# Performance work log

Hardware: AMD Instinct MI355X
Metric: run time of the kernel (lower is better)

The kernel has to match this reference:

```python
import jax, jax.numpy as jnp
import numpy as np

B, N, E, D = 4, 50000, 800000, 64


def setup_inputs() -> dict:
    key = jax.random.key(0)
    k_h, k_e, k_w1, k_w2 = jax.random.split(key, 4)
    s = 1.0 / np.sqrt(D)  # glorot-ish scale for 64x64 linear weights
    return {
        "t": jnp.zeros((1,), jnp.float32),
        "h": jax.random.normal(k_h, (B, N, D), jnp.float32),
        "edge_index": jax.random.randint(k_e, (2, E), 0, N, jnp.int32),
        "W1": jax.random.normal(k_w1, (D, D), jnp.float32) * s,
        "b1": jnp.zeros((D,), jnp.float32),
        "W2": jax.random.normal(k_w2, (D, D), jnp.float32) * s,
        "b2": jnp.zeros((D,), jnp.float32),
    }


def _gcn(x, row, col, norm, W, b, n_nodes):
    # x: (B, N, D). PyG GCNConv: linear (no bias) -> normalized gather/scatter -> +bias
    xw = jnp.einsum("bnd,de->bne", x, W)
    msg = xw[:, row, :] * norm[None, :, None]          # (B, E+N, D)
    agg = jax.vmap(lambda m: jax.ops.segment_sum(m, col, num_segments=n_nodes))(msg)
    return agg + b


def reference(t, h, edge_index, W1, b1, W2, b2):
    n_nodes = h.shape[1]
    loop = jnp.arange(n_nodes, dtype=edge_index.dtype)
    # add self-loops (PyG GCNConv default)
    row = jnp.concatenate([edge_index[0], loop])  # source nodes
    col = jnp.concatenate([edge_index[1], loop])  # target nodes
    # symmetric normalization D^{-1/2} (A+I) D^{-1/2}; degree counted on targets
    deg = jax.ops.segment_sum(jnp.ones_like(row, dtype=h.dtype), col, num_segments=n_nodes)
    dis = jnp.where(deg > 0, jax.lax.rsqrt(deg), 0.0)
    norm = dis[row] * dis[col]
    h = jnp.tanh(_gcn(h, row, col, norm, W1, b1, n_nodes))
    h = jnp.tanh(_gcn(h, row, col, norm, W2, b2, n_nodes))
    return h
```

## Files before the change

kernel.cpp:

```cpp
#include <hip/hip_runtime.h>
#include <math.h>

#define B_ 4
#define N_ 50000
#define E_ 800000
#define D_ 64
#define M_ (B_*N_)

#define LIN_BLKS_ (M_/64)
#define FILL_BLKS_ ((E_+255)/256)
#define CNT_BLKS_ ((E_/4+255)/256)

typedef _Float16 h4 __attribute__((ext_vector_type(4)));
typedef _Float16 h8 __attribute__((ext_vector_type(8)));
typedef float    f4 __attribute__((ext_vector_type(4)));

__device__ __forceinline__ void wfrag_one(const float* __restrict__ W, h8* __restrict__ Wf, int fid) {
  int khalf = fid >> 8, rem = fid & 255, tt = rem >> 6, lane = rem & 63;
  int kq = lane >> 4, m = lane & 15;
  h8 v;
#pragma unroll
  for (int j = 0; j < 8; j++) {
    int k = khalf * 32 + kq * 8 + j;
    v[j] = (_Float16)W[k * 64 + tt * 16 + m];
  }
  Wf[fid] = v;
}

__global__ __launch_bounds__(256) void k_count(const int4* __restrict__ col4, int* __restrict__ cnt,
                                               const float* __restrict__ W1, const float* __restrict__ W2,
                                               h8* __restrict__ Wf1, h8* __restrict__ Wf2) {
  if (blockIdx.x >= CNT_BLKS_) {
    int fa = (blockIdx.x - CNT_BLKS_) * 256 + threadIdx.x;
    if (fa < 512) wfrag_one(W1, Wf1, fa);
    else          wfrag_one(W2, Wf2, fa - 512);
    return;
  }
  int e = blockIdx.x * 256 + threadIdx.x;
  if (e < E_ / 4) {
    int4 c = col4[e];
    atomicAdd(&cnt[c.x], 1);
    atomicAdd(&cnt[c.y], 1);
    atomicAdd(&cnt[c.z], 1);
    atomicAdd(&cnt[c.w], 1);
  }
}

__global__ __launch_bounds__(1024) void k_scan(const int* __restrict__ cnt,
                                               float* __restrict__ dis,
                                               int* __restrict__ off, int* __restrict__ cur,
                                               int* __restrict__ gbase) {
  __shared__ int sd[1024];
  __shared__ int base_s;
  int i = blockIdx.x * 1024 + threadIdx.x;
  int v = (i < N_) ? cnt[i] : 0;
  if (i < N_) dis[i] = 1.0f / sqrtf((float)(v + 1));
  sd[threadIdx.x] = v;
  __syncthreads();
  for (int s = 1; s < 1024; s <<= 1) {
    int t = (threadIdx.x >= s) ? sd[threadIdx.x - s] : 0;
    __syncthreads();
    sd[threadIdx.x] += t;
    __syncthreads();
  }
  if (threadIdx.x == 1023) base_s = atomicAdd(gbase, sd[1023]);
  __syncthreads();
  if (i < N_) {
    off[i] = base_s + sd[threadIdx.x] - v;
    cur[i] = 0;
  }
}

template<int IN_F16>
__device__ __forceinline__ void linear_wave(const void* __restrict__ Xv, const h8* __restrict__ Wf,
                                            _Float16* __restrict__ Y, int wv, int lane) {
  int m = lane & 15, kq = lane >> 4;
  size_t r0 = (size_t)wv * 16;
  h8 a0, a1;
  if constexpr (IN_F16) {
    const _Float16* xr = (const _Float16*)Xv + (r0 + m) * 64 + kq * 8;
    a0 = *(const h8*)(xr);
    a1 = *(const h8*)(xr + 32);
  } else {
    const float* xr = (const float*)Xv + (r0 + m) * 64 + kq * 8;
    f4 f0 = *(const f4*)(xr);
    f4 f1 = *(const f4*)(xr + 4);
    f4 f2 = *(const f4*)(xr + 32);
    f4 f3 = *(const f4*)(xr + 36);
#pragma unroll
    for (int j = 0; j < 4; j++) {
      a0[j] = (_Float16)f0[j]; a0[j + 4] = (_Float16)f1[j];
      a1[j] = (_Float16)f2[j]; a1[j + 4] = (_Float16)f3[j];
    }
  }
  f4 acc[4];
#pragma unroll
  for (int t = 0; t < 4; t++) {
    h8 b0 = Wf[t * 64 + lane];
    h8 b1 = Wf[256 + t * 64 + lane];
    f4 c = {0.f, 0.f, 0.f, 0.f};
    c = __builtin_amdgcn_mfma_f32_16x16x32_f16(a0, b0, c, 0, 0, 0);
    c = __builtin_amdgcn_mfma_f32_16x16x32_f16(a1, b1, c, 0, 0, 0);
    acc[t] = c;
  }
  int b  = (int)(r0 / N_);
  int n0 = (int)(r0 - (size_t)b * N_);
#pragma unroll
  for (int t = 0; t < 4; t++) {
#pragma unroll
    for (int r = 0; r < 4; r++) {
      int n = n0 + kq * 4 + r;
      Y[(size_t)n * 256 + b * 64 + t * 16 + m] = (_Float16)acc[t][r];
    }
  }
}

__global__ __launch_bounds__(256) void k_fill_lin1(const int* __restrict__ row, const int* __restrict__ col,
                                                   const int* __restrict__ off, int* __restrict__ cur,
                                                   const float* __restrict__ dis, int2* __restrict__ em,
                                                   const float* __restrict__ h, const h8* __restrict__ Wf1,
                                                   _Float16* __restrict__ xw) {
  if (blockIdx.x < LIN_BLKS_) {
    int wv = blockIdx.x * 4 + (threadIdx.x >> 6);
    linear_wave<0>(h, Wf1, xw, wv, threadIdx.x & 63);
    return;
  }
  int e = (blockIdx.x - LIN_BLKS_) * 256 + threadIdx.x;
  if (e < E_) {
    int c = col[e], r = row[e];
    int p = off[c] + atomicAdd(&cur[c], 1);
    float w = dis[r] * dis[c];
    em[p] = make_int2(r << 9, __float_as_int(w));
  }
}

__global__ __launch_bounds__(256) void k_linear2(const _Float16* __restrict__ X, const h8* __restrict__ Wf,
                                                 _Float16* __restrict__ Y) {
  int wv = blockIdx.x * 4 + (threadIdx.x >> 6);
  linear_wave<1>(X, Wf, Y, wv, threadIdx.x & 63);
}

template<int OUT_F16>
__global__ __launch_bounds__(512) void k_agg(const _Float16* __restrict__ xw,
                                             const int* __restrict__ off,
                                             const int* __restrict__ cnt,
                                             const int2* __restrict__ em,
                                             const float* __restrict__ bias,
                                             void* __restrict__ outv) {
  int node = blockIdx.x * 8 + (threadIdx.x >> 6);
  int lane = threadIdx.x & 63;
  const char* xb = (const char*)xw + (size_t)(lane * 8);
  int s0  = __builtin_amdgcn_readfirstlane(off[node]);
  int deg = __builtin_amdgcn_readfirstlane(cnt[node]);
  int e0  = s0 + deg;
  float sw = 1.0f / (float)(deg + 1);
  h4 sv = *(const h4*)(xb + ((size_t)node << 9));
  f4 acc = __builtin_convertvector(sv, f4) * sw;
#define EDGE_(mm) do { \
    h4 v_ = *(const h4*)(xb + (unsigned)(mm).x); \
    acc += __builtin_convertvector(v_, f4) * __int_as_float((mm).y); \
  } while (0)
  int j = s0;
  for (; j + 8 <= e0; j += 8) {
    int2 m0 = em[j],     m1 = em[j + 1], m2 = em[j + 2], m3 = em[j + 3];
    int2 m4 = em[j + 4], m5 = em[j + 5], m6 = em[j + 6], m7 = em[j + 7];
    EDGE_(m0); EDGE_(m1); EDGE_(m2); EDGE_(m3);
    EDGE_(m4); EDGE_(m5); EDGE_(m6); EDGE_(m7);
  }
  for (; j < e0; ++j) { int2 mm = em[j]; EDGE_(mm); }
#undef EDGE_
  int b  = lane >> 4;
  int d0 = (lane & 15) * 4;
  f4 bb = *(const f4*)(bias + d0);
  float r0 = tanhf(acc.x + bb.x);
  float r1 = tanhf(acc.y + bb.y);
  float r2 = tanhf(acc.z + bb.z);
  float r3 = tanhf(acc.w + bb.w);
  if constexpr (OUT_F16) {
    h4 o;
    o[0] = (_Float16)r0; o[1] = (_Float16)r1;
    o[2] = (_Float16)r2; o[3] = (_Float16)r3;
    *(h4*)((_Float16*)outv + ((size_t)b * N_ + node) * 64 + d0) = o;
  } else {
    f4 r = {r0, r1, r2, r3};
    *(f4*)((float*)outv + ((size_t)b * N_ + node) * 64 + d0) = r;
  }
}

extern "C" void kernel_launch(void* const* d_in, const int* in_sizes, int n_in,
                              void* d_out, int out_size, void* d_ws, size_t ws_size,
                              hipStream_t stream) {
  const float* h  = (const float*)d_in[1];
  const int*   ei = (const int*)d_in[2];
  const float* W1 = (const float*)d_in[3];
  const float* b1 = (const float*)d_in[4];
  const float* W2 = (const float*)d_in[5];
  const float* b2 = (const float*)d_in[6];
  float* out = (float*)d_out;
  const int* row = ei;
  const int* col = ei + E_;

  char* p = (char*)d_ws;
  _Float16* xw = (_Float16*)p; p += (size_t)M_ * D_ * sizeof(_Float16);
  int2* em  = (int2*)p;   p += (size_t)E_ * sizeof(int2);
  int*  cnt = (int*)p;    p += (size_t)N_ * sizeof(int);
  int*  gbase = (int*)p;  p += 4 * sizeof(int);
  int*  off = (int*)p;    p += (size_t)N_ * sizeof(int);
  int*  cur = (int*)p;    p += (size_t)N_ * sizeof(int);
  float* dis = (float*)p; p += (size_t)N_ * sizeof(float);
  h8*   Wf1 = (h8*)p;     p += 512 * sizeof(h8);
  h8*   Wf2 = (h8*)p;     p += 512 * sizeof(h8);
  _Float16* h1 = (_Float16*)d_out;

  hipMemsetAsync(cnt, 0, (N_ + 4) * sizeof(int), stream);

  k_count<<<CNT_BLKS_ + 4, 256, 0, stream>>>((const int4*)col, cnt, W1, W2, Wf1, Wf2);
  k_scan<<<(N_ + 1023) / 1024, 1024, 0, stream>>>(cnt, dis, off, cur, gbase);
  k_fill_lin1<<<LIN_BLKS_ + FILL_BLKS_, 256, 0, stream>>>(row, col, off, cur, dis, em, h, Wf1, xw);
  k_agg<1><<<N_ / 8, 512, 0, stream>>>(xw, off, cnt, em, b1, h1);
  k_linear2<<<M_ / 64, 256, 0, stream>>>(h1, Wf2, xw);
  k_agg<0><<<N_ / 8, 512, 0, stream>>>(xw, off, cnt, em, b2, out);
}
```

Measured before the change: 326.1 us.

## Reuse count atomics as CSR ranks and aggregate two nodes per wave

```diff
diff --git a/kernel.cpp b/kernel.cpp
--- a/kernel.cpp
+++ b/kernel.cpp
@@ -28,6 +28,7 @@
 }
 
 __global__ __launch_bounds__(256) void k_count(const int4* __restrict__ col4, int* __restrict__ cnt,
+                                               int4* __restrict__ rank4,
                                                const float* __restrict__ W1, const float* __restrict__ W2,
                                                h8* __restrict__ Wf1, h8* __restrict__ Wf2) {
   if (blockIdx.x >= CNT_BLKS_) {
@@ -39,17 +40,18 @@
   int e = blockIdx.x * 256 + threadIdx.x;
   if (e < E_ / 4) {
     int4 c = col4[e];
-    atomicAdd(&cnt[c.x], 1);
-    atomicAdd(&cnt[c.y], 1);
-    atomicAdd(&cnt[c.z], 1);
-    atomicAdd(&cnt[c.w], 1);
+    int4 r;
+    r.x = atomicAdd(&cnt[c.x], 1);
+    r.y = atomicAdd(&cnt[c.y], 1);
+    r.z = atomicAdd(&cnt[c.z], 1);
+    r.w = atomicAdd(&cnt[c.w], 1);
+    rank4[e] = r;
   }
 }
 
 __global__ __launch_bounds__(1024) void k_scan(const int* __restrict__ cnt,
                                                float* __restrict__ dis,
-                                               int* __restrict__ off, int* __restrict__ cur,
-                                               int* __restrict__ gbase) {
+                                               int* __restrict__ off, int* __restrict__ gbase) {
   __shared__ int sd[1024];
   __shared__ int base_s;
   int i = blockIdx.x * 1024 + threadIdx.x;
@@ -65,10 +67,7 @@
   }
   if (threadIdx.x == 1023) base_s = atomicAdd(gbase, sd[1023]);
   __syncthreads();
-  if (i < N_) {
-    off[i] = base_s + sd[threadIdx.x] - v;
-    cur[i] = 0;
-  }
+  if (i < N_) off[i] = base_s + sd[threadIdx.x] - v;
 }
 
 template<int IN_F16>
@@ -116,7 +115,7 @@
 }
 
 __global__ __launch_bounds__(256) void k_fill_lin1(const int* __restrict__ row, const int* __restrict__ col,
-                                                   const int* __restrict__ off, int* __restrict__ cur,
+                                                   const int* __restrict__ off, const int* __restrict__ rank,
                                                    const float* __restrict__ dis, int2* __restrict__ em,
                                                    const float* __restrict__ h, const h8* __restrict__ Wf1,
                                                    _Float16* __restrict__ xw) {
@@ -128,7 +127,7 @@
   int e = (blockIdx.x - LIN_BLKS_) * 256 + threadIdx.x;
   if (e < E_) {
     int c = col[e], r = row[e];
-    int p = off[c] + atomicAdd(&cur[c], 1);
+    int p = off[c] + rank[e];
     float w = dis[r] * dis[c];
     em[p] = make_int2(r << 9, __float_as_int(w));
   }
@@ -147,44 +146,98 @@
                                              const int2* __restrict__ em,
                                              const float* __restrict__ bias,
                                              void* __restrict__ outv) {
-  int node = blockIdx.x * 8 + (threadIdx.x >> 6);
+  int wid  = blockIdx.x * 8 + (threadIdx.x >> 6);
   int lane = threadIdx.x & 63;
+  int na = wid * 2, nb = na + 1;
   const char* xb = (const char*)xw + (size_t)(lane * 8);
-  int s0  = __builtin_amdgcn_readfirstlane(off[node]);
-  int deg = __builtin_amdgcn_readfirstlane(cnt[node]);
-  int e0  = s0 + deg;
-  float sw = 1.0f / (float)(deg + 1);
-  h4 sv = *(const h4*)(xb + ((size_t)node << 9));
-  f4 acc = __builtin_convertvector(sv, f4) * sw;
-#define EDGE_(mm) do { \
+  int sa = __builtin_amdgcn_readfirstlane(off[na]);
+  int da = __builtin_amdgcn_readfirstlane(cnt[na]);
+  int sb = __builtin_amdgcn_readfirstlane(off[nb]);
+  int db = __builtin_amdgcn_readfirstlane(cnt[nb]);
+  int ea = sa + da, eb = sb + db;
+  float swa = 1.0f / (float)(da + 1);
+  float swb = 1.0f / (float)(db + 1);
+  h4 sva = *(const h4*)(xb + ((size_t)na << 9));
+  h4 svb = *(const h4*)(xb + ((size_t)nb << 9));
+  f4 acca = __builtin_convertvector(sva, f4) * swa;
+  f4 accb = __builtin_convertvector(svb, f4) * swb;
+#define EDGE_(mm, acc) do { \
     h4 v_ = *(const h4*)(xb + (unsigned)(mm).x); \
     acc += __builtin_convertvector(v_, f4) * __int_as_float((mm).y); \
   } while (0)
-  int j = s0;
-  for (; j + 8 <= e0; j += 8) {
-    int2 m0 = em[j],     m1 = em[j + 1], m2 = em[j + 2], m3 = em[j + 3];
-    int2 m4 = em[j + 4], m5 = em[j + 5], m6 = em[j + 6], m7 = em[j + 7];
-    EDGE_(m0); EDGE_(m1); EDGE_(m2); EDGE_(m3);
-    EDGE_(m4); EDGE_(m5); EDGE_(m6); EDGE_(m7);
-  }
-  for (; j < e0; ++j) { int2 mm = em[j]; EDGE_(mm); }
+#define BATCH8_(j, acc) do { \
+    int2 m0 = em[j],     m1 = em[(j)+1], m2 = em[(j)+2], m3 = em[(j)+3]; \
+    int2 m4 = em[(j)+4], m5 = em[(j)+5], m6 = em[(j)+6], m7 = em[(j)+7]; \
+    EDGE_(m0, acc); EDGE_(m1, acc); EDGE_(m2, acc); EDGE_(m3, acc); \
+    EDGE_(m4, acc); EDGE_(m5, acc); EDGE_(m6, acc); EDGE_(m7, acc); \
+  } while (0)
+  int ja = sa, jb = sb;
+  while (ja + 8 <= ea && jb + 8 <= eb) {
+    int2 a0 = em[ja],     a1 = em[ja + 1], a2 = em[ja + 2], a3 = em[ja + 3];
+    int2 a4 = em[ja + 4], a5 = em[ja + 5], a6 = em[ja + 6], a7 = em[ja + 7];
+    int2 b0 = em[jb],     b1 = em[jb + 1], b2 = em[jb + 2], b3 = em[jb + 3];
+    int2 b4 = em[jb + 4], b5 = em[jb + 5], b6 = em[jb + 6], b7 = em[jb + 7];
+    h4 va0 = *(const h4*)(xb + (unsigned)a0.x);
+    h4 va1 = *(const h4*)(xb + (unsigned)a1.x);
+    h4 va2 = *(const h4*)(xb + (unsigned)a2.x);
+    h4 va3 = *(const h4*)(xb + (unsigned)a3.x);
+    h4 va4 = *(const h4*)(xb + (unsigned)a4.x);
+    h4 va5 = *(const h4*)(xb + (unsigned)a5.x);
+    h4 va6 = *(const h4*)(xb + (unsigned)a6.x);
+    h4 va7 = *(const h4*)(xb + (unsigned)a7.x);
+    h4 vb0 = *(const h4*)(xb + (unsigned)b0.x);
+    h4 vb1 = *(const h4*)(xb + (unsigned)b1.x);
+    h4 vb2 = *(const h4*)(xb + (unsigned)b2.x);
+    h4 vb3 = *(const h4*)(xb + (unsigned)b3.x);
+    h4 vb4 = *(const h4*)(xb + (unsigned)b4.x);
+    h4 vb5 = *(const h4*)(xb + (unsigned)b5.x);
+    h4 vb6 = *(const h4*)(xb + (unsigned)b6.x);
+    h4 vb7 = *(const h4*)(xb + (unsigned)b7.x);
+    acca += __builtin_convertvector(va0, f4) * __int_as_float(a0.y);
+    acca += __builtin_convertvector(va1, f4) * __int_as_float(a1.y);
+    acca += __builtin_convertvector(va2, f4) * __int_as_float(a2.y);
+    acca += __builtin_convertvector(va3, f4) * __int_as_float(a3.y);
+    acca += __builtin_convertvector(va4, f4) * __int_as_float(a4.y);
+    acca += __builtin_convertvector(va5, f4) * __int_as_float(a5.y);
+    acca += __builtin_convertvector(va6, f4) * __int_as_float(a6.y);
+    acca += __builtin_convertvector(va7, f4) * __int_as_float(a7.y);
+    accb += __builtin_convertvector(vb0, f4) * __int_as_float(b0.y);
+    accb += __builtin_convertvector(vb1, f4) * __int_as_float(b1.y);
+    accb += __builtin_convertvector(vb2, f4) * __int_as_float(b2.y);
+    accb += __builtin_convertvector(vb3, f4) * __int_as_float(b3.y);
+    accb += __builtin_convertvector(vb4, f4) * __int_as_float(b4.y);
+    accb += __builtin_convertvector(vb5, f4) * __int_as_float(b5.y);
+    accb += __builtin_convertvector(vb6, f4) * __int_as_float(b6.y);
+    accb += __builtin_convertvector(vb7, f4) * __int_as_float(b7.y);
+    ja += 8; jb += 8;
+  }
+  while (ja + 8 <= ea) { BATCH8_(ja, acca); ja += 8; }
+  while (jb + 8 <= eb) { BATCH8_(jb, accb); jb += 8; }
+  for (; ja < ea; ++ja) { int2 mm = em[ja]; EDGE_(mm, acca); }
+  for (; jb < eb; ++jb) { int2 mm = em[jb]; EDGE_(mm, accb); }
+#undef BATCH8_
 #undef EDGE_
   int b  = lane >> 4;
   int d0 = (lane & 15) * 4;
   f4 bb = *(const f4*)(bias + d0);
-  float r0 = tanhf(acc.x + bb.x);
-  float r1 = tanhf(acc.y + bb.y);
-  float r2 = tanhf(acc.z + bb.z);
-  float r3 = tanhf(acc.w + bb.w);
-  if constexpr (OUT_F16) {
-    h4 o;
-    o[0] = (_Float16)r0; o[1] = (_Float16)r1;
-    o[2] = (_Float16)r2; o[3] = (_Float16)r3;
-    *(h4*)((_Float16*)outv + ((size_t)b * N_ + node) * 64 + d0) = o;
-  } else {
-    f4 r = {r0, r1, r2, r3};
-    *(f4*)((float*)outv + ((size_t)b * N_ + node) * 64 + d0) = r;
-  }
+#define STORE_(acc, node) do { \
+    float r0 = tanhf((acc).x + bb.x); \
+    float r1 = tanhf((acc).y + bb.y); \
+    float r2 = tanhf((acc).z + bb.z); \
+    float r3 = tanhf((acc).w + bb.w); \
+    if constexpr (OUT_F16) { \
+      h4 o; \
+      o[0] = (_Float16)r0; o[1] = (_Float16)r1; \
+      o[2] = (_Float16)r2; o[3] = (_Float16)r3; \
+      *(h4*)((_Float16*)outv + ((size_t)b * N_ + (node)) * 64 + d0) = o; \
+    } else { \
+      f4 r = {r0, r1, r2, r3}; \
+      *(f4*)((float*)outv + ((size_t)b * N_ + (node)) * 64 + d0) = r; \
+    } \
+  } while (0)
+  STORE_(acca, na);
+  STORE_(accb, nb);
+#undef STORE_
 }
 
 extern "C" void kernel_launch(void* const* d_in, const int* in_sizes, int n_in,
@@ -203,10 +256,10 @@
   char* p = (char*)d_ws;
   _Float16* xw = (_Float16*)p; p += (size_t)M_ * D_ * sizeof(_Float16);
   int2* em  = (int2*)p;   p += (size_t)E_ * sizeof(int2);
+  int*  rank = (int*)p;   p += (size_t)E_ * sizeof(int);
   int*  cnt = (int*)p;    p += (size_t)N_ * sizeof(int);
   int*  gbase = (int*)p;  p += 4 * sizeof(int);
   int*  off = (int*)p;    p += (size_t)N_ * sizeof(int);
-  int*  cur = (int*)p;    p += (size_t)N_ * sizeof(int);
   float* dis = (float*)p; p += (size_t)N_ * sizeof(float);
   h8*   Wf1 = (h8*)p;     p += 512 * sizeof(h8);
   h8*   Wf2 = (h8*)p;     p += 512 * sizeof(h8);
@@ -214,10 +267,10 @@
 
   hipMemsetAsync(cnt, 0, (N_ + 4) * sizeof(int), stream);
 
-  k_count<<<CNT_BLKS_ + 4, 256, 0, stream>>>((const int4*)col, cnt, W1, W2, Wf1, Wf2);
-  k_scan<<<(N_ + 1023) / 1024, 1024, 0, stream>>>(cnt, dis, off, cur, gbase);
-  k_fill_lin1<<<LIN_BLKS_ + FILL_BLKS_, 256, 0, stream>>>(row, col, off, cur, dis, em, h, Wf1, xw);
-  k_agg<1><<<N_ / 8, 512, 0, stream>>>(xw, off, cnt, em, b1, h1);
+  k_count<<<CNT_BLKS_ + 4, 256, 0, stream>>>((const int4*)col, cnt, (int4*)rank, W1, W2, Wf1, Wf2);
+  k_scan<<<(N_ + 1023) / 1024, 1024, 0, stream>>>(cnt, dis, off, gbase);
+  k_fill_lin1<<<LIN_BLKS_ + FILL_BLKS_, 256, 0, stream>>>(row, col, off, rank, dis, em, h, Wf1, xw);
+  k_agg<1><<<N_ / 16, 512, 0, stream>>>(xw, off, cnt, em, b1, h1);
   k_linear2<<<M_ / 64, 256, 0, stream>>>(h1, Wf2, xw);
-  k_agg<0><<<N_ / 8, 512, 0, stream>>>(xw, off, cnt, em, b2, out);
-}
+  k_agg<0><<<N_ / 16, 512, 0, stream>>>(xw, off, cnt, em, b2, out);
+}
```

New measurement: 312.0 us. 4.3% less time.
